# Optimization experiments

Hardware: AMD Instinct MI355X
Metric: run time of the kernel (lower is better)

Reference implementation:

```python
import jax, jax.numpy as jnp
import numpy as np

# 7 axial hex directions (dy, dx) including center, matching HexConv2d.DIRS
DIRS = [(0, 0), (1, 0), (0, 1), (-1, 1), (-1, 0), (0, -1), (1, -1)]


def _shift(x, dy, dx):
    """torch.roll-style shift with zero fill at wrapped edges. x: [B,C,H,W]."""
    sx, sy = -dx, -dy
    y = jnp.roll(x, shift=(sy, sx), axis=(2, 3))
    if sy > 0:
        y = y.at[:, :, :sy, :].set(0)
    elif sy < 0:
        y = y.at[:, :, sy:, :].set(0)
    if sx > 0:
        y = y.at[:, :, :, :sx].set(0)
    elif sx < 0:
        y = y.at[:, :, :, sx:].set(0)
    return y


def _hex_mask(H, dtype):
    size = H // 2
    q = jnp.arange(-size, size + 1)
    Q, R = jnp.meshgrid(q, q, indexing='ij')
    S = -Q - R
    # |Q|<=size and |R|<=size hold by construction; only |S|<=size cuts corners
    mask = ((jnp.abs(Q) <= size) & (jnp.abs(R) <= size) & (jnp.abs(S) <= size))
    return mask.astype(dtype)[None, None]  # [1,1,H,W]


def setup_inputs() -> dict:
    key = jax.random.key(0)
    k1, k2, k3 = jax.random.split(key, 3)
    B, Cin, Cout, H = 32, 256, 256, 49
    x = jax.random.normal(k1, (B, Cin, H, H), dtype=jnp.float32)
    weight = jax.random.normal(k2, (Cout, Cin, 7), dtype=jnp.float32) * 0.02
    bias = jax.random.normal(k3, (Cout,), dtype=jnp.float32) * 0.02
    return {"x": x, "weight": weight, "bias": bias}


def reference(x, weight, bias):
    mask = _hex_mask(x.shape[2], x.dtype)          # [1,1,H,W]
    x = x * mask
    # [7,B,C,H,W]: shifted+masked neighbor maps
    nbr = jnp.stack([_shift(x, dy, dx) for (dy, dx) in DIRS], axis=0) * mask
    # fused 1x1 conv over (channel, direction): weight [O,C,7]
    y = jnp.einsum('nbchw,ocn->bohw', nbr, weight) + bias[None, :, None, None]
    return y * mask
```

## Files before the change

### kernel.cpp

```cpp
#include <hip/hip_runtime.h>


typedef __attribute__((ext_vector_type(8))) short short8;
typedef __attribute__((ext_vector_type(4))) short short4v;
typedef __attribute__((ext_vector_type(4))) float floatx4;

#define NPIX   2401
#define W50    50
#define PREAL  2450
#define XBLEAD 56
#define XBROWS 2672
#define PT6    160
#define NT6    16
#define NSEG6  17
#define BUF6   (2*NSEG6*1024)
#define XB3_BYTES ((size_t)32*XBROWS*256*2)
#define WP_BYTES  917504ULL
#define WS_NEED3  (XB3_BYTES + WP_BYTES)
#define NPADROW 271

__device__ __forceinline__ unsigned short f2bf(float f) {
  unsigned u = __builtin_bit_cast(unsigned, f);
  u += 0x7fffu + ((u >> 16) & 1u);
  return (unsigned short)(u >> 16);
}

__global__ void prep_w_kernel(const float* __restrict__ w, unsigned short* __restrict__ wp) {
  int t = blockIdx.x * 256 + threadIdx.x;
  int l  = t & 63;
  int ot = (t >> 6) & 15;
  int kc = (t >> 10) & 7;
  int n  = t >> 13;
  int o  = ot * 16 + (l & 15);
  int cb = kc * 32 + ((l >> 4) * 8);
  const float* src = w + (size_t)(o * 256 + cb) * 7 + n;
  short8 pk;
#pragma unroll
  for (int j = 0; j < 8; ++j) pk[j] = (short)f2bf(src[j * 7]);
  ((short8*)wp)[t] = pk;
}

__global__ void zero_pads5(unsigned short* __restrict__ xb) {
  int idx = blockIdx.x * 256 + threadIdx.x;
  if (idx >= 32 * NPADROW * 32) return;
  int c16 = idx & 31;
  int rr  = idx >> 5;
  int pr  = rr % NPADROW;
  int b   = rr / NPADROW;
  int row;
  if (pr < 56)        row = pr;
  else if (pr < 105)  row = 105 + 50 * (pr - 56);
  else                row = 2506 + (pr - 105);
  short8 z = {0,0,0,0,0,0,0,0};
  *(short8*)(xb + ((size_t)b * XBROWS + row) * 256 + c16 * 8) = z;
}

__global__ __launch_bounds__(256)
void prep_x4(const float* __restrict__ x, unsigned short* __restrict__ xb) {
  __shared__ unsigned short t[64][68];
  const int tid = threadIdx.x;
  const int span = blockIdx.x, cg = blockIdx.y, b = blockIdx.z;
  const int s0 = span * 64;
  {
    const int chl = tid >> 2, i4 = tid & 3;
    const float* src = x + ((size_t)(b * 256 + cg * 64 + chl)) * NPIX;
    const int rbase = s0 + i4 * 16;
#pragma unroll
    for (int it = 0; it < 4; ++it) {
      int r = rbase + it * 4;
      float vv[4] = {0.f, 0.f, 0.f, 0.f};
      if (r + 3 < NPIX) {
        float4 v = *(const float4*)(src + r);
        vv[0] = v.x; vv[1] = v.y; vv[2] = v.z; vv[3] = v.w;
      } else {
#pragma unroll
        for (int e = 0; e < 4; ++e) if (r + e < NPIX) vv[e] = src[r + e];
      }
      short4v u = {0, 0, 0, 0};
#pragma unroll
      for (int e = 0; e < 4; ++e) {
        int re = r + e;
        unsigned short uu = 0;
        if (re < NPIX) {
          int h = re / 49, w = re - h * 49, s = h + w;
          if (s >= 24 && s <= 72) uu = f2bf(vv[e]);
        }
        u[e] = (short)uu;
      }
      *(short4v*)&t[chl][i4 * 16 + it * 4] = u;
    }
  }
  __syncthreads();
  const int pp = tid >> 3;
  const int co = tid & 7;
  unsigned d[8];
#pragma unroll
  for (int k = 0; k < 8; ++k) d[k] = *(const unsigned*)&t[co * 8 + k][pp * 2];
  uint4 lo, hi;
  {
    unsigned l0[4], h0[4];
#pragma unroll
    for (int m = 0; m < 4; ++m) {
      unsigned a = d[2 * m], bq = d[2 * m + 1];
      l0[m] = (a & 0xffffu) | (bq << 16);
      h0[m] = (a >> 16) | (bq & 0xffff0000u);
    }
    lo = make_uint4(l0[0], l0[1], l0[2], l0[3]);
    hi = make_uint4(h0[0], h0[1], h0[2], h0[3]);
  }
  const int r_lo = s0 + pp * 2, r_hi = r_lo + 1;
  if (r_lo < NPIX) {
    int prow = r_lo + r_lo / 49 + XBLEAD;
    *(uint4*)(xb + ((size_t)b * XBROWS + prow) * 256 + cg * 64 + co * 8) = lo;
  }
  if (r_hi < NPIX) {
    int prow = r_hi + r_hi / 49 + XBLEAD;
    *(uint4*)(xb + ((size_t)b * XBROWS + prow) * 256 + cg * 64 + co * 8) = hi;
  }
}

__global__ __launch_bounds__(256, 2)
void hexconv_v8(const unsigned short* __restrict__ xb,
                const unsigned short* __restrict__ wp,
                const float* __restrict__ bias,
                float* __restrict__ out) {
  __shared__ __attribute__((aligned(16))) unsigned char smem[2 * BUF6];

  const int tid  = threadIdx.x;
  const int lane = tid & 63;
  const int wv   = tid >> 6;
  const int col  = lane & 15;
  const int quad = lane >> 4;

  const int pt = blockIdx.x;
  const int b  = blockIdx.y;
  const int P0 = pt * PT6;
  const int phase = ((pt + b) & 3) * 2;

  const int OFF[7] = {0, 50, 1, -49, -50, -1, 49};

  unsigned pk[4];
  {
    int bav[7];
#pragma unroll
    for (int n = 0; n < 7; ++n) {
      int r0 = col + 56 + OFF[n];
      int r64 = r0 << 6;
      bav[n] = (r64 + quad * 16) ^ ((r64 >> 3) & 0x30);
    }
    pk[0] = (unsigned)bav[0] | ((unsigned)bav[1] << 16);
    pk[1] = (unsigned)bav[2] | ((unsigned)bav[3] << 16);
    pk[2] = (unsigned)bav[4] | ((unsigned)bav[5] << 16);
    pk[3] = (unsigned)bav[6];
  }

  const int gpart = (lane & 3) ^ ((lane >> 3) & 3);
  const char* gsrc0 = (const char*)(xb + ((size_t)b * XBROWS + (size_t)P0) * 256)
                      + (lane >> 2) * 512 + gpart * 16;

  auto stage2 = [&](int buf, int kc0) {
    char* ldsb = (char*)smem + buf * BUF6;
    for (int u = wv; u < 2 * NSEG6; u += 4) {
      int kk = (u >= NSEG6) ? 1 : 0;
      int s  = u - kk * NSEG6;
      __builtin_amdgcn_global_load_lds(
          (const __attribute__((address_space(1))) unsigned int*)
              (gsrc0 + (size_t)s * 8192 + (kc0 + kk) * 64),
          (__attribute__((address_space(3))) unsigned int*)(ldsb + u * 1024), 16, 0, 0);
    }
  };

  const char* wbase = (const char*)wp + (size_t)(wv * 4) * 1024 + lane * 16;

  floatx4 acc[4][10];
#pragma unroll
  for (int ii = 0; ii < 4; ++ii)
#pragma unroll
    for (int j = 0; j < 10; ++j) acc[ii][j] = (floatx4){0.f, 0.f, 0.f, 0.f};

  stage2(0, phase);
  __syncthreads();

  for (int i = 0; i < 4; ++i) {
    const int kc0  = (2 * i + phase) & 7;
    const int kc0n = (2 * i + 2 + phase) & 7;
    if (i < 3) stage2((i + 1) & 1, kc0n);
    const char* bufp = (const char*)smem + (i & 1) * BUF6;
#pragma unroll
    for (int n = 0; n < 7; ++n) {
      const int ban = (n & 1) ? (int)(pk[n >> 1] >> 16) : (int)(pk[n >> 1] & 0xffffu);
#pragma unroll
      for (int kk = 0; kk < 2; ++kk) {
        const int kc = kc0 + kk;
        short8 af[4];
#pragma unroll
        for (int ii = 0; ii < 4; ++ii)
          af[ii] = *(const short8*)(wbase + ((size_t)((n * 8 + kc) * 16 + ii)) * 1024);
        const char* bp = bufp + kk * (NSEG6 * 1024) + ban;
#pragma unroll
        for (int j = 0; j < 10; ++j) {
          short8 bf = *(const short8*)(bp + j * 1024);
#pragma unroll
          for (int ii = 0; ii < 4; ++ii)
            acc[ii][j] = __builtin_amdgcn_mfma_f32_16x16x32_bf16(af[ii], bf, acc[ii][j], 0, 0, 0);
        }
      }
    }
    if (i < 3) __syncthreads();
  }

  const int ob = wv * 64;
#pragma unroll
  for (int ii = 0; ii < 4; ++ii) {
    floatx4 bv = *(const floatx4*)(bias + ob + ii * 16 + quad * 4);
#pragma unroll
    for (int j = 0; j < 10; ++j)
#pragma unroll
      for (int rr = 0; rr < 4; ++rr) acc[ii][j][rr] += bv[rr];
  }

#pragma unroll
  for (int j = 0; j < 10; ++j) {
    int p = P0 + j * 16 + col;
    int h = p / W50;
    int w = p - h * W50;
    if (w >= 49 || p >= PREAL) continue;
    bool m = (h + w >= 24) && (h + w <= 72);
    int ridx = h * 49 + w;
#pragma unroll
    for (int ii = 0; ii < 4; ++ii) {
      int base = (b * 256 + ob + ii * 16 + quad * 4) * NPIX + ridx;
      float* dst = out + base;
#pragma unroll
      for (int rr = 0; rr < 4; ++rr) {
        float v = m ? acc[ii][j][rr] : 0.f;
        dst[rr * NPIX] = v;
      }
    }
  }
}

#define PITCH  40
#define V1WIN  168
#define V1ZROW 168
__global__ __launch_bounds__(256)
void hexconv_v1(const float* __restrict__ x,
                const unsigned short* __restrict__ wp,
                const float* __restrict__ bias,
                float* __restrict__ out) {
  __shared__ unsigned short sm[(V1ZROW + 2) * PITCH];
  const int tid = threadIdx.x, lane = tid & 63, wv = tid >> 6;
  const int col = lane & 15, quad = lane >> 4;
  const int pt = blockIdx.x, b = blockIdx.y;
  const int P0 = pt * 64, win_start = P0 - 52;
  if (tid < PITCH * 2) sm[V1ZROW * PITCH + tid] = 0;
  const int OFF[7] = {0, 49, 1, -48, -49, -1, 48};
  const int DXP = (1 << 2) | (1 << 3), DXN = (1 << 5) | (1 << 6);
  int baddr[4][7];
#pragma unroll
  for (int j = 0; j < 4; ++j) {
    int pix = P0 + j * 16 + col;
    int wj = pix % 49;
    int rowbase = pix - win_start;
#pragma unroll
    for (int n = 0; n < 7; ++n) {
      bool bad = (((DXP >> n) & 1) && wj == 48) || (((DXN >> n) & 1) && wj == 0);
      int row = bad ? V1ZROW : (rowbase + OFF[n]);
      baddr[j][n] = row * (PITCH * 2) + quad * 16;
    }
  }
  int sp[3], sgp[3]; bool sok[3];
#pragma unroll
  for (int pi = 0; pi < 3; ++pi) {
    int p = lane + pi * 64, gp = win_start + p;
    sp[pi] = p; sgp[pi] = gp;
    bool hm = false;
    if (gp >= 0 && gp < NPIX) { int h = gp / 49, w = gp - h * 49, s = h + w; hm = (s >= 24 && s <= 72); }
    sok[pi] = (p < V1WIN) && hm;
  }
  floatx4 acc[4][4];
#pragma unroll
  for (int i = 0; i < 4; ++i)
#pragma unroll
    for (int j = 0; j < 4; ++j) acc[i][j] = (floatx4){0.f, 0.f, 0.f, 0.f};
  const short8* wpv = (const short8*)wp;
  const int wslot = wv * 4;
  for (int kc = 0; kc < 8; ++kc) {
    __syncthreads();
#pragma unroll
    for (int ci = 0; ci < 8; ++ci) {
      int c = ci * 4 + wv;
      const float* src = x + ((size_t)(b * 256 + kc * 32 + c)) * NPIX;
#pragma unroll
      for (int pi = 0; pi < 3; ++pi) {
        if (sp[pi] < V1WIN) {
          float v = sok[pi] ? src[sgp[pi]] : 0.f;
          sm[sp[pi] * PITCH + c] = f2bf(v);
        }
      }
    }
    __syncthreads();
#pragma unroll
    for (int n = 0; n < 7; ++n) {
      short8 af[4];
#pragma unroll
      for (int i = 0; i < 4; ++i)
        af[i] = wpv[((size_t)((n * 8 + kc) * 16 + wslot + i)) * 64 + lane];
      short8 bf[4];
#pragma unroll
      for (int j = 0; j < 4; ++j)
        bf[j] = *(const short8*)((const char*)sm + baddr[j][n]);
#pragma unroll
      for (int i = 0; i < 4; ++i)
#pragma unroll
        for (int j = 0; j < 4; ++j)
          acc[i][j] = __builtin_amdgcn_mfma_f32_16x16x32_bf16(af[i], bf[j], acc[i][j], 0, 0, 0);
    }
  }
  const int ob = wv * 64;
  floatx4 bv[4];
#pragma unroll
  for (int i = 0; i < 4; ++i)
    bv[i] = *(const floatx4*)(bias + ob + i * 16 + quad * 4);
#pragma unroll
  for (int j = 0; j < 4; ++j) {
    int pix = P0 + j * 16 + col;
    if (pix >= NPIX) continue;
    int h = pix / 49, w = pix - h * 49;
    bool m = (h + w >= 24 && h + w <= 72);
#pragma unroll
    for (int i = 0; i < 4; ++i) {
      int o = ob + i * 16 + quad * 4;
      float* dst = out + ((size_t)(b * 256 + o)) * NPIX + pix;
#pragma unroll
      for (int r = 0; r < 4; ++r) {
        float v = m ? (acc[i][j][r] + bv[i][r]) : 0.f;
        dst[(size_t)r * NPIX] = v;
      }
    }
  }
}

extern "C" void kernel_launch(void* const* d_in, const int* in_sizes, int n_in,
                              void* d_out, int out_size, void* d_ws, size_t ws_size,
                              hipStream_t stream) {
  const float* x    = (const float*)d_in[0];
  const float* w    = (const float*)d_in[1];
  const float* bias = (const float*)d_in[2];
  float* out = (float*)d_out;

  if (ws_size >= WS_NEED3) {
    unsigned short* xb = (unsigned short*)d_ws;
    unsigned short* wp = (unsigned short*)((char*)d_ws + XB3_BYTES);
    zero_pads5<<<(32 * NPADROW * 32 + 255) / 256, 256, 0, stream>>>(xb);
    prep_w_kernel<<<224, 256, 0, stream>>>(w, wp);
    prep_x4<<<dim3(38, 4, 32), 256, 0, stream>>>(x, xb);
    hexconv_v8<<<dim3(NT6, 32), 256, 0, stream>>>(xb, wp, bias, out);
  } else {
    unsigned short* wp = (unsigned short*)d_ws;
    prep_w_kernel<<<224, 256, 0, stream>>>(w, wp);
    hexconv_v1<<<dim3(38, 32), 256, 0, stream>>>(x, wp, bias, out);
  }
}
```

Baseline: 229.5 us.

## Restructure hex conv into 512-thread persistent blocks with full-K LDS staging

Replaces the 256-thread kernel with a 512-thread block that stages all 8 K-chunks of a 160-pixel tile into LDS at once. Eight waves split the work as 4 output groups by 2 pixel halves. Each block handles two tiles, and the second tile's loads are issued before the first tile's epilogue so global loads overlap the stores. It also batches the B-fragment LDS reads before the MFMA burst and raises wave priority around the MFMAs. The costs are a much larger LDS footprint (about 139 KB per block), which may limit occupancy, and a grid of only 256 blocks.

Result: slower. 580.0 us (+152.7%).

```diff
diff --git a/kernel.cpp b/kernel.cpp
--- a/kernel.cpp
+++ b/kernel.cpp
@@ -11,9 +11,9 @@
 #define XBLEAD 56
 #define XBROWS 2672
 #define PT6    160
-#define NT6    16
 #define NSEG6  17
-#define BUF6   (2*NSEG6*1024)
+#define KCOL9  (NSEG6*1024)
+#define LDS9   (8*KCOL9)
 #define XB3_BYTES ((size_t)32*XBROWS*256*2)
 #define WP_BYTES  917504ULL
 #define WS_NEED3  (XB3_BYTES + WP_BYTES)
@@ -119,123 +119,133 @@
   }
 }
 
-__global__ __launch_bounds__(256, 2)
-void hexconv_v8(const unsigned short* __restrict__ xb,
+__global__ __launch_bounds__(512, 2)
+void hexconv_v9(const unsigned short* __restrict__ xb,
                 const unsigned short* __restrict__ wp,
                 const float* __restrict__ bias,
                 float* __restrict__ out) {
-  __shared__ __attribute__((aligned(16))) unsigned char smem[2 * BUF6];
+  __shared__ __attribute__((aligned(16))) unsigned char smem[LDS9];
 
   const int tid  = threadIdx.x;
   const int lane = tid & 63;
   const int wv   = tid >> 6;
   const int col  = lane & 15;
   const int quad = lane >> 4;
-
-  const int pt = blockIdx.x;
+  const int oh   = wv >> 1;
+  const int ph   = wv & 1;
+
+  const int bx = blockIdx.x;
   const int b  = blockIdx.y;
-  const int P0 = pt * PT6;
-  const int phase = ((pt + b) & 3) * 2;
 
   const int OFF[7] = {0, 50, 1, -49, -50, -1, 49};
 
-  unsigned pk[4];
+  int ba[7];
+#pragma unroll
+  for (int n = 0; n < 7; ++n) {
+    int r0 = col + 56 + OFF[n];
+    int r64 = r0 << 6;
+    ba[n] = ((r64 + quad * 16) ^ ((r64 >> 3) & 0x30)) + ph * 5120;
+  }
+
+  const int gpart = (lane & 3) ^ ((lane >> 3) & 3);
+  const int lrow  = lane >> 2;
+
+  const char* wbase = (const char*)wp + (size_t)(oh * 4) * 1024 + lane * 16;
+
+  floatx4 acc[4][5];
+#pragma unroll
+  for (int ii = 0; ii < 4; ++ii)
+#pragma unroll
+    for (int j = 0; j < 5; ++j) acc[ii][j] = (floatx4){0.f, 0.f, 0.f, 0.f};
+
   {
-    int bav[7];
-#pragma unroll
-    for (int n = 0; n < 7; ++n) {
-      int r0 = col + 56 + OFF[n];
-      int r64 = r0 << 6;
-      bav[n] = (r64 + quad * 16) ^ ((r64 >> 3) & 0x30);
-    }
-    pk[0] = (unsigned)bav[0] | ((unsigned)bav[1] << 16);
-    pk[1] = (unsigned)bav[2] | ((unsigned)bav[3] << 16);
-    pk[2] = (unsigned)bav[4] | ((unsigned)bav[5] << 16);
-    pk[3] = (unsigned)bav[6];
-  }
-
-  const int gpart = (lane & 3) ^ ((lane >> 3) & 3);
-  const char* gsrc0 = (const char*)(xb + ((size_t)b * XBROWS + (size_t)P0) * 256)
-                      + (lane >> 2) * 512 + gpart * 16;
-
-  auto stage2 = [&](int buf, int kc0) {
-    char* ldsb = (char*)smem + buf * BUF6;
-    for (int u = wv; u < 2 * NSEG6; u += 4) {
-      int kk = (u >= NSEG6) ? 1 : 0;
-      int s  = u - kk * NSEG6;
+    const char* gsrc0 = (const char*)xb
+        + ((size_t)b * XBROWS + (size_t)bx * PT6) * 512 + lrow * 512 + gpart * 16;
+    for (int u = wv; u < 8 * NSEG6; u += 8) {
+      int kc = u / NSEG6;
+      int s  = u - kc * NSEG6;
       __builtin_amdgcn_global_load_lds(
           (const __attribute__((address_space(1))) unsigned int*)
-              (gsrc0 + (size_t)s * 8192 + (kc0 + kk) * 64),
-          (__attribute__((address_space(3))) unsigned int*)(ldsb + u * 1024), 16, 0, 0);
-    }
-  };
-
-  const char* wbase = (const char*)wp + (size_t)(wv * 4) * 1024 + lane * 16;
-
-  floatx4 acc[4][10];
-#pragma unroll
-  for (int ii = 0; ii < 4; ++ii)
-#pragma unroll
-    for (int j = 0; j < 10; ++j) acc[ii][j] = (floatx4){0.f, 0.f, 0.f, 0.f};
-
-  stage2(0, phase);
+              (gsrc0 + (size_t)s * 8192 + kc * 64),
+          (__attribute__((address_space(3))) unsigned int*)(smem + u * 1024), 16, 0, 0);
+    }
+  }
   __syncthreads();
 
-  for (int i = 0; i < 4; ++i) {
-    const int kc0  = (2 * i + phase) & 7;
-    const int kc0n = (2 * i + 2 + phase) & 7;
-    if (i < 3) stage2((i + 1) & 1, kc0n);
-    const char* bufp = (const char*)smem + (i & 1) * BUF6;
+#pragma unroll 1
+  for (int tt = 0; tt < 2; ++tt) {
 #pragma unroll
     for (int n = 0; n < 7; ++n) {
-      const int ban = (n & 1) ? (int)(pk[n >> 1] >> 16) : (int)(pk[n >> 1] & 0xffffu);
-#pragma unroll
-      for (int kk = 0; kk < 2; ++kk) {
-        const int kc = kc0 + kk;
+#pragma unroll
+      for (int kc = 0; kc < 8; ++kc) {
         short8 af[4];
 #pragma unroll
         for (int ii = 0; ii < 4; ++ii)
-          af[ii] = *(const short8*)(wbase + ((size_t)((n * 8 + kc) * 16 + ii)) * 1024);
-        const char* bp = bufp + kk * (NSEG6 * 1024) + ban;
-#pragma unroll
-        for (int j = 0; j < 10; ++j) {
-          short8 bf = *(const short8*)(bp + j * 1024);
+          af[ii] = *(const short8*)(wbase + (size_t)((n * 8 + kc) * 16 + ii) * 1024);
+        const char* bp = (const char*)smem + kc * KCOL9 + ba[n];
+        short8 bfv[5];
+#pragma unroll
+        for (int j = 0; j < 5; ++j)
+          bfv[j] = *(const short8*)(bp + j * 1024);
+        __builtin_amdgcn_s_setprio(1);
+#pragma unroll
+        for (int j = 0; j < 5; ++j)
 #pragma unroll
           for (int ii = 0; ii < 4; ++ii)
-            acc[ii][j] = __builtin_amdgcn_mfma_f32_16x16x32_bf16(af[ii], bf, acc[ii][j], 0, 0, 0);
+            acc[ii][j] = __builtin_amdgcn_mfma_f32_16x16x32_bf16(af[ii], bfv[j], acc[ii][j], 0, 0, 0);
+        __builtin_amdgcn_s_setprio(0);
+      }
+    }
+    __syncthreads();
+
+    if (tt == 0) {
+      const char* gsrc1 = (const char*)xb
+          + ((size_t)b * XBROWS + (size_t)(bx + 8) * PT6) * 512 + lrow * 512 + gpart * 16;
+      for (int u = wv; u < 8 * NSEG6; u += 8) {
+        int kc = u / NSEG6;
+        int s  = u - kc * NSEG6;
+        __builtin_amdgcn_global_load_lds(
+            (const __attribute__((address_space(1))) unsigned int*)
+                (gsrc1 + (size_t)s * 8192 + kc * 64),
+            (__attribute__((address_space(3))) unsigned int*)(smem + u * 1024), 16, 0, 0);
+      }
+    }
+
+    const int P0 = (bx + 8 * tt) * PT6;
+    const int ob = oh * 64;
+#pragma unroll
+    for (int ii = 0; ii < 4; ++ii) {
+      floatx4 bv = *(const floatx4*)(bias + ob + ii * 16 + quad * 4);
+#pragma unroll
+      for (int j = 0; j < 5; ++j)
+#pragma unroll
+        for (int rr = 0; rr < 4; ++rr) acc[ii][j][rr] += bv[rr];
+    }
+#pragma unroll
+    for (int j = 0; j < 5; ++j) {
+      int p = P0 + ph * 80 + j * 16 + col;
+      int h = p / W50;
+      int w = p - h * W50;
+      if (w >= 49 || p >= PREAL) continue;
+      bool m = (h + w >= 24) && (h + w <= 72);
+      int ridx = h * 49 + w;
+#pragma unroll
+      for (int ii = 0; ii < 4; ++ii) {
+        float* dst = out + ((b * 256 + ob + ii * 16 + quad * 4) * NPIX + ridx);
+#pragma unroll
+        for (int rr = 0; rr < 4; ++rr) {
+          float v = m ? acc[ii][j][rr] : 0.f;
+          dst[rr * NPIX] = v;
         }
       }
     }
-    if (i < 3) __syncthreads();
-  }
-
-  const int ob = wv * 64;
-#pragma unroll
-  for (int ii = 0; ii < 4; ++ii) {
-    floatx4 bv = *(const floatx4*)(bias + ob + ii * 16 + quad * 4);
-#pragma unroll
-    for (int j = 0; j < 10; ++j)
-#pragma unroll
-      for (int rr = 0; rr < 4; ++rr) acc[ii][j][rr] += bv[rr];
-  }
-
-#pragma unroll
-  for (int j = 0; j < 10; ++j) {
-    int p = P0 + j * 16 + col;
-    int h = p / W50;
-    int w = p - h * W50;
-    if (w >= 49 || p >= PREAL) continue;
-    bool m = (h + w >= 24) && (h + w <= 72);
-    int ridx = h * 49 + w;
-#pragma unroll
-    for (int ii = 0; ii < 4; ++ii) {
-      int base = (b * 256 + ob + ii * 16 + quad * 4) * NPIX + ridx;
-      float* dst = out + base;
-#pragma unroll
-      for (int rr = 0; rr < 4; ++rr) {
-        float v = m ? acc[ii][j][rr] : 0.f;
-        dst[rr * NPIX] = v;
-      }
+
+    if (tt == 0) {
+#pragma unroll
+      for (int ii = 0; ii < 4; ++ii)
+#pragma unroll
+        for (int j = 0; j < 5; ++j) acc[ii][j] = (floatx4){0.f, 0.f, 0.f, 0.f};
+      __syncthreads();
     }
   }
 }
@@ -355,7 +365,7 @@
     zero_pads5<<<(32 * NPADROW * 32 + 255) / 256, 256, 0, stream>>>(xb);
     prep_w_kernel<<<224, 256, 0, stream>>>(w, wp);
     prep_x4<<<dim3(38, 4, 32), 256, 0, stream>>>(x, xb);
-    hexconv_v8<<<dim3(NT6, 32), 256, 0, stream>>>(xb, wp, bias, out);
+    hexconv_v9<<<dim3(8, 32), 512, 0, stream>>>(xb, wp, bias, out);
   } else {
     unsigned short* wp = (unsigned short*)d_ws;
     prep_w_kernel<<<224, 256, 0, stream>>>(w, wp);
```
